# Optimization experiments

Measured on AMD Instinct MI355X. Metric: run time of the kernel, lower is better.

The kernel has to match this reference:

```python
import jax, jax.numpy as jnp
import numpy as np

B, N, D, E = 8, 512, 64, 32

def setup_inputs() -> dict:
    key = jax.random.key(0)
    k1, k2, k3 = jax.random.split(key, 3)
    x = jax.random.normal(k1, (B, N, D), dtype=jnp.float32)
    We = jax.random.normal(k2, (2 * D, E), dtype=jnp.float32) * (1.0 / np.sqrt(2 * D))
    be = jnp.zeros((E,), dtype=jnp.float32)
    Wr = jax.random.normal(k3, (N * E, 1), dtype=jnp.float32) * (1.0 / np.sqrt(N * E))
    br = jnp.zeros((1,), dtype=jnp.float32)
    return {"x": x, "We": We, "be": be, "Wr": Wr, "br": br}

def reference(x, We, be, Wr, br):
    b, n, d = x.shape
    # cat([x_i, x_j]) @ We == x_i @ We[:d] + x_j @ We[d:]  (avoids materializing the concat)
    W_src, W_dst = We[:d], We[d:]
    src = jnp.einsum('bid,de->bie', x, W_src)   # [B,N,E] contribution of start node i
    dst = jnp.einsum('bjd,de->bje', x, W_dst)   # [B,N,E] contribution of terminal node j
    edges = jax.nn.relu(src[:, :, None, :] + dst[:, None, :, :] + be)  # [B,N,N,E] edge (i->j)
    incoming = jnp.swapaxes(edges, 1, 2)        # [B, N(dst), N(src), E] permute(0,2,1,3)
    agg = incoming.reshape(b, n, n * edges.shape[-1])  # [B,N,N*E]
    delta = agg @ Wr + br                       # [B,N,1]
    return delta
```

## Files before the change

kernel.cpp:

```cpp
#include <hip/hip_runtime.h>


__global__ __launch_bounds__(256) void proj_kernel(
    const float* __restrict__ x, const float* __restrict__ We,
    const float* __restrict__ be, const float* __restrict__ br,
    float* __restrict__ out, float* __restrict__ ws)
{
    const int tid  = threadIdx.x;
    const int pe   = tid & 63;
    const int rloc = tid >> 6;
    const int row  = blockIdx.x * 4 + rloc;
    const int proj = pe >> 5;
    const int e    = pe & 31;

    const float* __restrict__ xrow = x + (size_t)row * 64;
    const float* __restrict__ wcol = We + proj * (64 * 32) + e;

    float acc = 0.0f;
    #pragma unroll
    for (int d = 0; d < 64; ++d)
        acc = fmaf(xrow[d], wcol[d * 32], acc);

    if (proj == 0) acc += be[e];

    ws[(size_t)proj * (4096 * 32) + (size_t)row * 32 + e] = acc;

    const int gid = blockIdx.x * 256 + tid;
    if (gid < 4096) out[gid] = br[0];
}

__global__ __launch_bounds__(256) void edge_kernel(
    const float* __restrict__ ws, const float* __restrict__ Wr,
    float* __restrict__ out)
{
    const float* __restrict__ src = ws;
    const float* __restrict__ dst = ws + 4096 * 32;

    const int b  = blockIdx.z;
    const int j  = blockIdx.y * 256 + threadIdx.x;
    const int i0 = blockIdx.x * 16;

    float d[32];
    const float4* __restrict__ dp =
        (const float4*)(dst + ((size_t)(b * 512 + j)) * 32);
    #pragma unroll
    for (int k = 0; k < 8; ++k) ((float4*)d)[k] = dp[k];

    float acc0 = 0.0f, acc1 = 0.0f;

    #pragma unroll 4
    for (int ii = 0; ii < 16; ++ii) {
        const int i = i0 + ii;
        const float* __restrict__ srow = src + ((size_t)(b * 512 + i)) * 32;
        const float* __restrict__ wrow = Wr + (size_t)i * 32;
        #pragma unroll
        for (int e = 0; e < 32; e += 2) {
            float t0 = fmaxf(srow[e]     + d[e],     0.0f);
            float t1 = fmaxf(srow[e + 1] + d[e + 1], 0.0f);
            acc0 = fmaf(t0, wrow[e],     acc0);
            acc1 = fmaf(t1, wrow[e + 1], acc1);
        }
    }

    atomicAdd(&out[b * 512 + j], acc0 + acc1);
}

extern "C" void kernel_launch(void* const* d_in, const int* in_sizes, int n_in,
                              void* d_out, int out_size, void* d_ws, size_t ws_size,
                              hipStream_t stream) {
    const float* x  = (const float*)d_in[0];
    const float* We = (const float*)d_in[1];
    const float* be = (const float*)d_in[2];
    const float* Wr = (const float*)d_in[3];
    const float* br = (const float*)d_in[4];
    float* out = (float*)d_out;
    float* ws  = (float*)d_ws;

    proj_kernel<<<1024, 256, 0, stream>>>(x, We, be, br, out, ws);
    edge_kernel<<<dim3(32, 2, 8), 256, 0, stream>>>(ws, Wr, out);
}
```

Before: 76.54 us.

## Register-block two destination nodes per thread in edge kernel, retile proj grid

Each edge-kernel thread now handles two destination nodes (j and j+256), so every src/Wr element it loads is reused across two accumulator pairs. The i-chunk per block drops from 16 to 8, giving 64x1x8 blocks in place of 32x2x8. The projection kernel is relaunched as one 64-thread block per row, replacing 4 rows per 256-thread block. This cuts redundant broadcast loads of src and Wr, at the cost of twice the register footprint for d and more atomics per output.

After: 73.31 us. 1.04x faster.

```diff
diff --git a/kernel.cpp b/kernel.cpp
--- a/kernel.cpp
+++ b/kernel.cpp
@@ -1,17 +1,16 @@
 #include <hip/hip_runtime.h>
 
+#define BNE (4096 * 32)
 
-__global__ __launch_bounds__(256) void proj_kernel(
+__global__ __launch_bounds__(64) void proj_kernel(
     const float* __restrict__ x, const float* __restrict__ We,
     const float* __restrict__ be, const float* __restrict__ br,
     float* __restrict__ out, float* __restrict__ ws)
 {
-    const int tid  = threadIdx.x;
-    const int pe   = tid & 63;
-    const int rloc = tid >> 6;
-    const int row  = blockIdx.x * 4 + rloc;
-    const int proj = pe >> 5;
-    const int e    = pe & 31;
+    const int lane = threadIdx.x;
+    const int row  = blockIdx.x;
+    const int proj = lane >> 5;
+    const int e    = lane & 31;
 
     const float* __restrict__ xrow = x + (size_t)row * 64;
     const float* __restrict__ wcol = We + proj * (64 * 32) + e;
@@ -23,10 +22,9 @@
 
     if (proj == 0) acc += be[e];
 
-    ws[(size_t)proj * (4096 * 32) + (size_t)row * 32 + e] = acc;
+    ws[(size_t)proj * BNE + (size_t)row * 32 + e] = acc;
 
-    const int gid = blockIdx.x * 256 + tid;
-    if (gid < 4096) out[gid] = br[0];
+    if (blockIdx.x < 64) out[blockIdx.x * 64 + lane] = br[0];
 }
 
 __global__ __launch_bounds__(256) void edge_kernel(
@@ -34,35 +32,46 @@
     float* __restrict__ out)
 {
     const float* __restrict__ src = ws;
-    const float* __restrict__ dst = ws + 4096 * 32;
+    const float* __restrict__ dst = ws + BNE;
 
     const int b  = blockIdx.z;
-    const int j  = blockIdx.y * 256 + threadIdx.x;
-    const int i0 = blockIdx.x * 16;
+    const int j0 = threadIdx.x;
+    const int j1 = threadIdx.x + 256;
+    const int i0 = blockIdx.x * 8;
 
-    float d[32];
-    const float4* __restrict__ dp =
-        (const float4*)(dst + ((size_t)(b * 512 + j)) * 32);
+    float d0[32], d1[32];
+    const float4* __restrict__ dp0 = (const float4*)(dst + ((size_t)(b * 512 + j0)) * 32);
+    const float4* __restrict__ dp1 = (const float4*)(dst + ((size_t)(b * 512 + j1)) * 32);
     #pragma unroll
-    for (int k = 0; k < 8; ++k) ((float4*)d)[k] = dp[k];
+    for (int k = 0; k < 8; ++k) {
+        ((float4*)d0)[k] = dp0[k];
+        ((float4*)d1)[k] = dp1[k];
+    }
 
-    float acc0 = 0.0f, acc1 = 0.0f;
+    float a00 = 0.f, a01 = 0.f, a10 = 0.f, a11 = 0.f;
 
-    #pragma unroll 4
-    for (int ii = 0; ii < 16; ++ii) {
+    #pragma unroll 2
+    for (int ii = 0; ii < 8; ++ii) {
         const int i = i0 + ii;
         const float* __restrict__ srow = src + ((size_t)(b * 512 + i)) * 32;
         const float* __restrict__ wrow = Wr + (size_t)i * 32;
         #pragma unroll
         for (int e = 0; e < 32; e += 2) {
-            float t0 = fmaxf(srow[e]     + d[e],     0.0f);
-            float t1 = fmaxf(srow[e + 1] + d[e + 1], 0.0f);
-            acc0 = fmaf(t0, wrow[e],     acc0);
-            acc1 = fmaf(t1, wrow[e + 1], acc1);
+            const float s0 = srow[e],  s1 = srow[e + 1];
+            const float w0 = wrow[e],  w1 = wrow[e + 1];
+            float t00 = fmaxf(s0 + d0[e],     0.f);
+            float t01 = fmaxf(s1 + d0[e + 1], 0.f);
+            float t10 = fmaxf(s0 + d1[e],     0.f);
+            float t11 = fmaxf(s1 + d1[e + 1], 0.f);
+            a00 = fmaf(t00, w0, a00);
+            a01 = fmaf(t01, w1, a01);
+            a10 = fmaf(t10, w0, a10);
+            a11 = fmaf(t11, w1, a11);
         }
     }
 
-    atomicAdd(&out[b * 512 + j], acc0 + acc1);
+    atomicAdd(&out[b * 512 + j0], a00 + a01);
+    atomicAdd(&out[b * 512 + j1], a10 + a11);
 }
 
 extern "C" void kernel_launch(void* const* d_in, const int* in_sizes, int n_in,
@@ -76,6 +85,6 @@
     float* out = (float*)d_out;
     float* ws  = (float*)d_ws;
 
-    proj_kernel<<<1024, 256, 0, stream>>>(x, We, be, br, out, ws);
-    edge_kernel<<<dim3(32, 2, 8), 256, 0, stream>>>(ws, Wr, out);
+    proj_kernel<<<4096, 64, 0, stream>>>(x, We, be, br, out, ws);
+    edge_kernel<<<dim3(64, 1, 8), 256, 0, stream>>>(ws, Wr, out);
 }
```
